# Kernel tuning notes

Measured on AMD Instinct MI355X. Metric: run time of the kernel, lower is better.

## Reference

```python
import jax, jax.numpy as jnp
import numpy as np

B, N, D, H = 2, 28, 128, 8
DK = D // H  # 16


def setup_inputs() -> dict:
    key0 = jax.random.key(0)
    ks = jax.random.split(key0, 10)
    query = jax.random.normal(ks[0], (B, N, N, D), dtype=jnp.float32)
    key = jax.random.normal(ks[1], (B, N, N, D), dtype=jnp.float32)
    value = jax.random.normal(ks[2], (B, N, N, D), dtype=jnp.float32)
    mask = jax.random.randint(ks[3], (B, N, N, N), 0, 2).astype(bool)
    scale = 1.0 / np.sqrt(D)
    # six bias-free Linear(d_model, d_model) weights (torch layout: y = x @ W.T)
    Wlk = jax.random.normal(ks[4], (D, D), dtype=jnp.float32) * scale
    Wrk = jax.random.normal(ks[5], (D, D), dtype=jnp.float32) * scale
    Wlv = jax.random.normal(ks[6], (D, D), dtype=jnp.float32) * scale
    Wrv = jax.random.normal(ks[7], (D, D), dtype=jnp.float32) * scale
    Wq = jax.random.normal(ks[8], (D, D), dtype=jnp.float32) * scale
    Wout = jax.random.normal(ks[9], (D, D), dtype=jnp.float32) * scale
    return {"query": query, "key": key, "value": value, "mask": mask,
            "Wlk": Wlk, "Wrk": Wrk, "Wlv": Wlv, "Wrv": Wrv, "Wq": Wq, "Wout": Wout}


def reference(query, key, value, mask, Wlk, Wrk, Wlv, Wrv, Wq, Wout):
    b, n = key.shape[0], key.shape[1]

    def proj(x, W):
        # torch nn.Linear(bias=False): x @ W.T, then view to heads
        return (x @ W.T).reshape(b, n, n, H, DK)

    left_k = proj(key, Wlk)
    right_k = proj(key, Wrk)
    left_v = proj(value, Wlv)
    right_v = proj(value, Wrv)
    # note: linears[4](key) (the 'query' projection, Wq) is computed in the
    # original but unused when lesion_scores=False; omitted (same math).

    # scores[b,x,a,y,h] = <left_k[b,x,a,h,:], right_k[b,a,y,h,:]> / sqrt(d_k)
    scores = jnp.einsum('bxahd,bayhd->bxayh', left_k, right_k) / np.float32(np.sqrt(DK))
    scores = jnp.where(mask[..., None], jnp.float32(-1e9), scores)
    att = jax.nn.softmax(scores, axis=2)  # softmax over intermediate node a
    # dropout p=0.0 -> identity
    # x[b,x,y,h,d] = sum_a att[b,x,a,y,h] * left_v[b,x,a,h,d] * right_v[b,a,y,h,d]
    x = jnp.einsum('bxayh,bxahd,bayhd->bxyhd', att, left_v, right_v)
    x = x.reshape(b, n, n, D)
    return x @ Wout.T
```

## Files before the change

kernel.cpp:

```cpp
#include <hip/hip_runtime.h>

#define B_ 2
#define N_ 28
#define D_ 128
#define H_ 8
#define DK_ 16
#define R_ (B_ * N_ * N_)
#define ROWS_PER_BLK 8

__global__ __launch_bounds__(128) void proj4_kernel(
    const float* __restrict__ key, const float* __restrict__ value,
    const float* __restrict__ Wlk, const float* __restrict__ Wrk,
    const float* __restrict__ Wlv, const float* __restrict__ Wrv,
    float* __restrict__ ws) {
  const int p = blockIdx.y;
  const float* X = (p < 2) ? key : value;
  const float* W = (p == 0) ? Wlk : (p == 1) ? Wrk : (p == 2) ? Wlv : Wrv;
  float* Y = ws + (size_t)p * R_ * D_;

  const int r0 = blockIdx.x * ROWS_PER_BLK;
  const int c = threadIdx.x;

  __shared__ __align__(16) float xs[ROWS_PER_BLK][D_];
#pragma unroll
  for (int i = 0; i < ROWS_PER_BLK; ++i)
    xs[i][c] = X[(size_t)(r0 + i) * D_ + c];
  __syncthreads();

  const float4* w4 = reinterpret_cast<const float4*>(W + (size_t)c * D_);
  float acc[ROWS_PER_BLK];
#pragma unroll
  for (int i = 0; i < ROWS_PER_BLK; ++i) acc[i] = 0.f;

#pragma unroll
  for (int k = 0; k < D_ / 4; ++k) {
    const float4 wv = w4[k];
#pragma unroll
    for (int i = 0; i < ROWS_PER_BLK; ++i) {
      const float4 xv = reinterpret_cast<const float4*>(xs[i])[k];
      acc[i] += xv.x * wv.x + xv.y * wv.y + xv.z * wv.z + xv.w * wv.w;
    }
  }

#pragma unroll
  for (int i = 0; i < ROWS_PER_BLK; ++i)
    Y[(size_t)(r0 + i) * D_ + c] = acc[i];
}

__global__ __launch_bounds__(128) void attn_out_kernel(
    const float* __restrict__ ws, const int* __restrict__ mask,
    const float* __restrict__ Wout, float* __restrict__ out) {
  const float* lk = ws;
  const float* rk = ws + (size_t)1 * R_ * D_;
  const float* lv = ws + (size_t)2 * R_ * D_;
  const float* rv = ws + (size_t)3 * R_ * D_;

  const int bxy = blockIdx.x;
  const int y = bxy % N_;
  const int bx = bxy / N_;
  const int b = bx / N_;
  const int tid = threadIdx.x;

  const int rowL = bx * N_;
  const int rowR = b * N_ * N_ + y;

  float s[N_];
#pragma unroll
  for (int a = 0; a < N_; ++a) {
    float pr = lk[(size_t)(rowL + a) * D_ + tid] *
               rk[(size_t)(rowR + a * N_) * D_ + tid];
    pr += __shfl_xor(pr, 1);
    pr += __shfl_xor(pr, 2);
    pr += __shfl_xor(pr, 4);
    pr += __shfl_xor(pr, 8);
    s[a] = pr * 0.25f;
  }

  const int* mrow = mask + (size_t)rowL * N_ + y;
#pragma unroll
  for (int a = 0; a < N_; ++a)
    if (mrow[(size_t)a * N_] != 0) s[a] = -1e9f;

  float mx = -3.0e38f;
#pragma unroll
  for (int a = 0; a < N_; ++a) mx = fmaxf(mx, s[a]);
  float den = 0.f;
#pragma unroll
  for (int a = 0; a < N_; ++a) {
    s[a] = __expf(s[a] - mx);
    den += s[a];
  }
  const float inv = 1.0f / den;

  float xv = 0.f;
#pragma unroll
  for (int a = 0; a < N_; ++a) {
    xv += s[a] * lv[(size_t)(rowL + a) * D_ + tid] *
          rv[(size_t)(rowR + a * N_) * D_ + tid];
  }

  __shared__ __align__(16) float s_x[D_];
  s_x[tid] = xv * inv;
  __syncthreads();

  const float4* wrow = reinterpret_cast<const float4*>(Wout + (size_t)tid * D_);
  const float4* x4 = reinterpret_cast<const float4*>(s_x);
  float acc = 0.f;
#pragma unroll
  for (int k = 0; k < D_ / 4; ++k) {
    const float4 xk = x4[k];
    const float4 wv = wrow[k];
    acc += xk.x * wv.x + xk.y * wv.y + xk.z * wv.z + xk.w * wv.w;
  }
  out[(size_t)bxy * D_ + tid] = acc;
}

extern "C" void kernel_launch(void* const* d_in, const int* in_sizes, int n_in,
                              void* d_out, int out_size, void* d_ws,
                              size_t ws_size, hipStream_t stream) {
  const float* key = (const float*)d_in[1];
  const float* value = (const float*)d_in[2];
  const int* mask = (const int*)d_in[3];
  const float* Wlk = (const float*)d_in[4];
  const float* Wrk = (const float*)d_in[5];
  const float* Wlv = (const float*)d_in[6];
  const float* Wrv = (const float*)d_in[7];
  const float* Wout = (const float*)d_in[9];
  float* out = (float*)d_out;
  float* ws = (float*)d_ws;

  proj4_kernel<<<dim3(R_ / ROWS_PER_BLK, 4), 128, 0, stream>>>(
      key, value, Wlk, Wrk, Wlv, Wrv, ws);
  attn_out_kernel<<<dim3(R_), 128, 0, stream>>>(ws, mask, Wout, out);
}
```

Before: 36.69 us.

## Pre-transpose weights and split output projection into a separate coalesced GEMM

Adds a kernel that transposes all five weight matrices into workspace so the projection GEMMs read weight rows coalesced as float4 across threads. Each thread now computes four output columns for one row, and key/value loads into shared memory are vectorised. The output projection moves out of the attention kernel into its own GEMM that uses the same layout. This adds two kernel launches and an extra round trip of the attention output through global memory, in exchange for avoiding strided per-thread weight reads.

```diff
diff --git a/kernel.cpp b/kernel.cpp
--- a/kernel.cpp
+++ b/kernel.cpp
@@ -8,48 +8,70 @@
 #define R_ (B_ * N_ * N_)
 #define ROWS_PER_BLK 8
 
-__global__ __launch_bounds__(128) void proj4_kernel(
-    const float* __restrict__ key, const float* __restrict__ value,
+#define WT_OFF (2u << 20)
+
+__global__ __launch_bounds__(256) void transposeW_kernel(
     const float* __restrict__ Wlk, const float* __restrict__ Wrk,
     const float* __restrict__ Wlv, const float* __restrict__ Wrv,
-    float* __restrict__ ws) {
+    const float* __restrict__ Wout, float* __restrict__ wt) {
+  const int wi = blockIdx.y;
+  const float* src = (wi == 0) ? Wlk
+                   : (wi == 1) ? Wrk
+                   : (wi == 2) ? Wlv
+                   : (wi == 3) ? Wrv : Wout;
+  float* dst = wt + (size_t)wi * D_ * D_;
+
+  const int tr = blockIdx.x >> 2;
+  const int tc = blockIdx.x & 3;
+  const int r0 = tr * 32, c0 = tc * 32;
+  const int tx = threadIdx.x;
+  const int ty = threadIdx.y;
+
+  __shared__ float t[32][33];
+#pragma unroll
+  for (int i = 0; i < 4; ++i)
+    t[ty + 8 * i][tx] = src[(size_t)(r0 + ty + 8 * i) * D_ + c0 + tx];
+  __syncthreads();
+#pragma unroll
+  for (int i = 0; i < 4; ++i)
+    dst[(size_t)(c0 + ty + 8 * i) * D_ + r0 + tx] = t[tx][ty + 8 * i];
+}
+
+__global__ __launch_bounds__(256) void proj4t_kernel(
+    const float* __restrict__ key, const float* __restrict__ value,
+    const float* __restrict__ wt, float* __restrict__ ws) {
   const int p = blockIdx.y;
   const float* X = (p < 2) ? key : value;
-  const float* W = (p == 0) ? Wlk : (p == 1) ? Wrk : (p == 2) ? Wlv : Wrv;
+  const float* Wt = wt + (size_t)p * D_ * D_;
   float* Y = ws + (size_t)p * R_ * D_;
 
   const int r0 = blockIdx.x * ROWS_PER_BLK;
-  const int c = threadIdx.x;
+  const int tid = threadIdx.x;
+  const int rr = tid >> 5;
+  const int cq = tid & 31;
 
   __shared__ __align__(16) float xs[ROWS_PER_BLK][D_];
-#pragma unroll
-  for (int i = 0; i < ROWS_PER_BLK; ++i)
-    xs[i][c] = X[(size_t)(r0 + i) * D_ + c];
+  reinterpret_cast<float4*>(xs[rr])[cq] =
+      reinterpret_cast<const float4*>(X + (size_t)(r0 + rr) * D_)[cq];
   __syncthreads();
 
-  const float4* w4 = reinterpret_cast<const float4*>(W + (size_t)c * D_);
-  float acc[ROWS_PER_BLK];
-#pragma unroll
-  for (int i = 0; i < ROWS_PER_BLK; ++i) acc[i] = 0.f;
-
-#pragma unroll
-  for (int k = 0; k < D_ / 4; ++k) {
-    const float4 wv = w4[k];
-#pragma unroll
-    for (int i = 0; i < ROWS_PER_BLK; ++i) {
-      const float4 xv = reinterpret_cast<const float4*>(xs[i])[k];
-      acc[i] += xv.x * wv.x + xv.y * wv.y + xv.z * wv.z + xv.w * wv.w;
-    }
+  const float* xrow = xs[rr];
+  float4 acc = {0.f, 0.f, 0.f, 0.f};
+#pragma unroll 8
+  for (int k = 0; k < D_; ++k) {
+    const float4 wv = reinterpret_cast<const float4*>(Wt + (size_t)k * D_)[cq];
+    const float xk = xrow[k];
+    acc.x += xk * wv.x;
+    acc.y += xk * wv.y;
+    acc.z += xk * wv.z;
+    acc.w += xk * wv.w;
   }
-
-#pragma unroll
-  for (int i = 0; i < ROWS_PER_BLK; ++i)
-    Y[(size_t)(r0 + i) * D_ + c] = acc[i];
+  reinterpret_cast<float4*>(Y + (size_t)(r0 + rr) * D_)[cq] = acc;
 }
 
-__global__ __launch_bounds__(128) void attn_out_kernel(
+__global__ __launch_bounds__(128) void attn_kernel(
     const float* __restrict__ ws, const int* __restrict__ mask,
-    const float* __restrict__ Wout, float* __restrict__ out) {
+    float* __restrict__ xout) {
   const float* lk = ws;
   const float* rk = ws + (size_t)1 * R_ * D_;
   const float* lv = ws + (size_t)2 * R_ * D_;
@@ -98,21 +120,35 @@
     xv += s[a] * lv[(size_t)(rowL + a) * D_ + tid] *
           rv[(size_t)(rowR + a * N_) * D_ + tid];
   }
+  xout[(size_t)bxy * D_ + tid] = xv * inv;
+}
 
-  __shared__ __align__(16) float s_x[D_];
-  s_x[tid] = xv * inv;
+__global__ __launch_bounds__(256) void gemm_outt_kernel(
+    const float* __restrict__ X, const float* __restrict__ wtOut,
+    float* __restrict__ Y) {
+  const int r0 = blockIdx.x * ROWS_PER_BLK;
+  const int tid = threadIdx.x;
+  const int rr = tid >> 5;
+  const int cq = tid & 31;
+
+  __shared__ __align__(16) float xs[ROWS_PER_BLK][D_];
+  reinterpret_cast<float4*>(xs[rr])[cq] =
+      reinterpret_cast<const float4*>(X + (size_t)(r0 + rr) * D_)[cq];
   __syncthreads();
 
-  const float4* wrow = reinterpret_cast<const float4*>(Wout + (size_t)tid * D_);
-  const float4* x4 = reinterpret_cast<const float4*>(s_x);
-  float acc = 0.f;
-#pragma unroll
-  for (int k = 0; k < D_ / 4; ++k) {
-    const float4 xk = x4[k];
-    const float4 wv = wrow[k];
-    acc += xk.x * wv.x + xk.y * wv.y + xk.z * wv.z + xk.w * wv.w;
+  const float* xrow = xs[rr];
+  float4 acc = {0.f, 0.f, 0.f, 0.f};
+#pragma unroll 8
+  for (int k = 0; k < D_; ++k) {
+    const float4 wv =
+        reinterpret_cast<const float4*>(wtOut + (size_t)k * D_)[cq];
+    const float xk = xrow[k];
+    acc.x += xk * wv.x;
+    acc.y += xk * wv.y;
+    acc.z += xk * wv.z;
+    acc.w += xk * wv.w;
   }
-  out[(size_t)bxy * D_ + tid] = acc;
+  reinterpret_cast<float4*>(Y + (size_t)(r0 + rr) * D_)[cq] = acc;
 }
 
 extern "C" void kernel_launch(void* const* d_in, const int* in_sizes, int n_in,
@@ -129,7 +165,14 @@
   float* out = (float*)d_out;
   float* ws = (float*)d_ws;
 
-  proj4_kernel<<<dim3(R_ / ROWS_PER_BLK, 4), 128, 0, stream>>>(
-      key, value, Wlk, Wrk, Wlv, Wrv, ws);
-  attn_out_kernel<<<dim3(R_), 128, 0, stream>>>(ws, mask, Wout, out);
+  float* xbuf = ws + (size_t)4 * R_ * D_;
+  float* wt = ws + (size_t)WT_OFF;
+
+  transposeW_kernel<<<dim3(16, 5), dim3(32, 8), 0, stream>>>(
+      Wlk, Wrk, Wlv, Wrv, Wout, wt);
+  proj4t_kernel<<<dim3(R_ / ROWS_PER_BLK, 4), 256, 0, stream>>>(
+      key, value, wt, ws);
+  attn_kernel<<<dim3(R_), 128, 0, stream>>>(ws, mask, xbuf);
+  gemm_outt_kernel<<<dim3(R_ / ROWS_PER_BLK), 256, 0, stream>>>(
+      xbuf, wt + (size_t)4 * D_ * D_, out);
 }
```

After: 42.84 us. +16.8%, slower.
